# Performance work log

Measured on AMD Instinct MI355X. Metric: run time of the kernel, lower is better.

The kernel has to match this reference:

```python
import jax, jax.numpy as jnp
import numpy as np

# Config (BERT-base with T5-style shared relative attention bias)
B, S, D, H, F, V, L = 16, 512, 768, 12, 3072, 30522, 12
DH = D // H
MAXREL = 128  # bias table has 2*MAXREL+1 = 257 buckets
EPS = 1e-12


def layer_norm(x, w, b):
    mu = jnp.mean(x, axis=-1, keepdims=True)
    var = jnp.mean(jnp.square(x - mu), axis=-1, keepdims=True)
    return (x - mu) * jax.lax.rsqrt(var + EPS) * w + b


def setup_inputs() -> dict:
    key = jax.random.key(0)
    ks = jax.random.split(key, 16)
    s = 0.02
    inp = {
        "input_ids": jax.random.randint(ks[0], (B, S), 0, V),
        "attention_mask": jnp.ones((B, S), jnp.float32),
        "word_emb": jax.random.normal(ks[1], (V, D), jnp.float32) * s,
        "pos_emb": jax.random.normal(ks[2], (S, D), jnp.float32) * s,
        "emb_ln_w": jnp.ones((D,), jnp.float32),
        "emb_ln_b": jnp.zeros((D,), jnp.float32),
        "rel_bias_table": jax.random.normal(ks[3], (2 * MAXREL + 1, H), jnp.float32) * s,
        "Wq": jax.random.normal(ks[4], (L, D, D), jnp.float32) * s,
        "bq": jnp.zeros((L, D), jnp.float32),
        "Wk": jax.random.normal(ks[5], (L, D, D), jnp.float32) * s,
        "bk": jnp.zeros((L, D), jnp.float32),
        "Wv": jax.random.normal(ks[6], (L, D, D), jnp.float32) * s,
        "bv": jnp.zeros((L, D), jnp.float32),
        "Wo": jax.random.normal(ks[7], (L, D, D), jnp.float32) * s,
        "bo": jnp.zeros((L, D), jnp.float32),
        "attn_ln_w": jnp.ones((L, D), jnp.float32),
        "attn_ln_b": jnp.zeros((L, D), jnp.float32),
        "Wi": jax.random.normal(ks[8], (L, F, D), jnp.float32) * s,
        "bi": jnp.zeros((L, F), jnp.float32),
        "Wd": jax.random.normal(ks[9], (L, D, F), jnp.float32) * s,
        "bd": jnp.zeros((L, D), jnp.float32),
        "out_ln_w": jnp.ones((L, D), jnp.float32),
        "out_ln_b": jnp.zeros((L, D), jnp.float32),
    }
    return inp


def _encoder(input_ids, attention_mask, word_emb, pos_emb, emb_ln_w, emb_ln_b,
             rel_bias_table, Wq, bq, Wk, bk, Wv, bv, Wo, bo, attn_ln_w, attn_ln_b,
             Wi, bi, Wd, bd, out_ln_w, out_ln_b):
    b, s = input_ids.shape
    # Embeddings: word + learned absolute position, then LayerNorm
    h = word_emb[input_ids] + pos_emb[:s][None, :, :]
    h = layer_norm(h, emb_ln_w, emb_ln_b)

    # Shared relative position bias: [H, S, S]
    pos = jnp.arange(s)
    rel = jnp.clip(pos[None, :] - pos[:, None], -MAXREL, MAXREL) + MAXREL
    rel_bias = jnp.transpose(rel_bias_table[rel], (2, 0, 1))[None]  # [1,H,S,S]

    # Additive attention mask: [B,1,1,S]
    add_mask = (1.0 - attention_mask)[:, None, None, :] * -10000.0
    scale = 1.0 / np.sqrt(DH)

    def step(h, p):
        wq, bq_, wk, bk_, wv, bv_, wo, bo_, lw1, lb1, wi, bi_, wd, bd_, lw2, lb2 = p
        q = (h @ wq.T + bq_).reshape(b, s, H, DH)
        k = (h @ wk.T + bk_).reshape(b, s, H, DH)
        v = (h @ wv.T + bv_).reshape(b, s, H, DH)
        scores = jnp.einsum('bqhd,bkhd->bhqk', q, k) * scale + rel_bias + add_mask
        attn = jax.nn.softmax(scores, axis=-1)
        ctx = jnp.einsum('bhqk,bkhd->bqhd', attn, v).reshape(b, s, D)
        h1 = layer_norm(h + (ctx @ wo.T + bo_), lw1, lb1)
        inter = jax.nn.gelu(h1 @ wi.T + bi_, approximate=False)
        h2 = layer_norm(h1 + (inter @ wd.T + bd_), lw2, lb2)
        return h2, None

    params = (Wq, bq, Wk, bk, Wv, bv, Wo, bo, attn_ln_w, attn_ln_b,
              Wi, bi, Wd, bd, out_ln_w, out_ln_b)
    h, _ = jax.lax.scan(step, h, params)
    return h


def reference(input_ids, attention_mask, word_emb, pos_emb, emb_ln_w, emb_ln_b,
              rel_bias_table, Wq, bq, Wk, bk, Wv, bv, Wo, bo, attn_ln_w, attn_ln_b,
              Wi, bi, Wd, bd, out_ln_w, out_ln_b):
    return _encoder(input_ids, attention_mask, word_emb, pos_emb, emb_ln_w, emb_ln_b,
                    rel_bias_table, Wq, bq, Wk, bk, Wv, bv, Wo, bo, attn_ln_w, attn_ln_b,
                    Wi, bi, Wd, bd, out_ln_w, out_ln_b)
```

## Files before the change

kernel.cpp:

```cpp
#include <hip/hip_runtime.h>
#include <cstdint>
#include <cstddef>

#define BB 16
#define SS 512
#define DD 768
#define HH 12
#define FF 3072
#define LL 12
#define DHD 64
#define MM (BB*SS)

typedef __attribute__((ext_vector_type(8))) short bf16x8;
typedef __attribute__((ext_vector_type(4))) float f32x4;

__device__ __forceinline__ ushort f2bf(float f) {
  union { float f; uint32_t u; } x; x.f = f;
  uint32_t r = x.u + 0x7FFFu + ((x.u >> 16) & 1u);
  return (ushort)(r >> 16);
}

__device__ __forceinline__ void glds16(const ushort* g, ushort* l) {
  __builtin_amdgcn_global_load_lds((__attribute__((address_space(1))) void*)g,
                                   (__attribute__((address_space(3))) void*)l,
                                   16, 0, 0);
}

__device__ __forceinline__ float gelu_t(float v) {
  float y = 0.7978845608f * (v + 0.044715f * v * v * v);
  y = fminf(fmaxf(y, -15.f), 15.f);
  float e = __expf(2.f * y);
  return 0.5f * v * (2.f - 2.f / (e + 1.f));
}

__global__ __launch_bounds__(256)
void convw6(const float* __restrict__ s0, const float* __restrict__ s1,
            const float* __restrict__ s2, const float* __restrict__ s3,
            const float* __restrict__ s4, const float* __restrict__ s5,
            ushort* __restrict__ dA, ushort* __restrict__ dB, int perD, int perF)
{
  const int y = blockIdx.y;
  const int per = (y < 4) ? perD : perF;
  const int i = (blockIdx.x * 256 + threadIdx.x) * 4;
  if (i >= per) return;
  const float* s = y == 0 ? s0 : y == 1 ? s1 : y == 2 ? s2 : y == 3 ? s3 : y == 4 ? s4 : s5;
  ushort* dst = (y < 4) ? (dA + (size_t)y * perD) : (dB + (size_t)(y - 4) * perF);
  const float4 v = *(const float4*)(s + i);
  ushort4 o;
  o.x = f2bf(v.x); o.y = f2bf(v.y); o.z = f2bf(v.z); o.w = f2bf(v.w);
  *(ushort4*)(dst + i) = o;
}

__global__ __launch_bounds__(256)
void embed_ln_kernel(const int* __restrict__ ids, const float* __restrict__ wemb,
                     const float* __restrict__ pemb, const float* __restrict__ g,
                     const float* __restrict__ bt, float* __restrict__ hf,
                     ushort* __restrict__ hb)
{
  const int row = blockIdx.x;
  const int s = row & (SS - 1);
  const int id = ids[row];
  const float* wp = wemb + (size_t)id * DD;
  const float* pp = pemb + (size_t)s * DD;
  const int tid = threadIdx.x;
  float v[3]; float sum = 0.f, sq = 0.f;
#pragma unroll
  for (int j = 0; j < 3; ++j) {
    int e = tid + j * 256;
    v[j] = wp[e] + pp[e];
    sum += v[j]; sq += v[j] * v[j];
  }
  __shared__ float red[2][4];
#pragma unroll
  for (int off = 32; off >= 1; off >>= 1) { sum += __shfl_xor(sum, off); sq += __shfl_xor(sq, off); }
  const int lane = tid & 63, wid = tid >> 6;
  if (lane == 0) { red[0][wid] = sum; red[1][wid] = sq; }
  __syncthreads();
  sum = red[0][0] + red[0][1] + red[0][2] + red[0][3];
  sq  = red[1][0] + red[1][1] + red[1][2] + red[1][3];
  const float mean = sum * (1.f / DD);
  const float var  = sq  * (1.f / DD) - mean * mean;
  const float rstd = rsqrtf(var + 1e-12f);
  const size_t base = (size_t)row * DD;
#pragma unroll
  for (int j = 0; j < 3; ++j) {
    int e = tid + j * 256;
    float o = (v[j] - mean) * rstd * g[e] + bt[e];
    hf[base + e] = o;
    hb[base + e] = f2bf(o);
  }
}

__global__ __launch_bounds__(256)
void add_ln2_kernel(const float* __restrict__ res, const float* __restrict__ p0,
                    const float* __restrict__ p1, const float* __restrict__ g,
                    const float* __restrict__ bt, float* __restrict__ hf,
                    ushort* __restrict__ hb)
{
  const int row = blockIdx.x;
  const int tid = threadIdx.x;
  const size_t base = (size_t)row * DD;
  float v[3]; float sum = 0.f, sq = 0.f;
#pragma unroll
  for (int j = 0; j < 3; ++j) {
    int e = tid + j * 256;
    v[j] = res[base + e] + p0[base + e] + p1[base + e];
    sum += v[j]; sq += v[j] * v[j];
  }
  __shared__ float red[2][4];
#pragma unroll
  for (int off = 32; off >= 1; off >>= 1) { sum += __shfl_xor(sum, off); sq += __shfl_xor(sq, off); }
  const int lane = tid & 63, wid = tid >> 6;
  if (lane == 0) { red[0][wid] = sum; red[1][wid] = sq; }
  __syncthreads();
  sum = red[0][0] + red[0][1] + red[0][2] + red[0][3];
  sq  = red[1][0] + red[1][1] + red[1][2] + red[1][3];
  const float mean = sum * (1.f / DD);
  const float var  = sq  * (1.f / DD) - mean * mean;
  const float rstd = rsqrtf(var + 1e-12f);
#pragma unroll
  for (int j = 0; j < 3; ++j) {
    int e = tid + j * 256;
    float o = (v[j] - mean) * rstd * g[e] + bt[e];
    hf[base + e] = o;
    hb[base + e] = f2bf(o);
  }
}

template<int EPI, bool TRV>
__global__ __launch_bounds__(256, 4)
void gemm_ker(const ushort* __restrict__ A,
              const ushort* __restrict__ B0, const ushort* __restrict__ B1,
              const ushort* __restrict__ B2,
              const float* __restrict__ bias0, const float* __restrict__ bias1,
              const float* __restrict__ bias2,
              void* __restrict__ C0, void* __restrict__ C1, void* __restrict__ C2,
              int Kdim, int nblk)
{
  __shared__ ushort As[2][128 * 32];
  __shared__ ushort Bs[2][128 * 32];

  int id = blockIdx.y * gridDim.x + blockIdx.x;
  const int chunk = (gridDim.x * gridDim.y) >> 3;
  id = (id & 7) * chunk + (id >> 3);
  const int bm = id & 63;
  const int bnAll = id >> 6;
  const int sub = bnAll / nblk;
  const int bn = bnAll - sub * nblk;

  const ushort* Bw  = sub == 0 ? B0 : (sub == 1 ? B1 : B2);
  const float* bias = sub == 0 ? bias0 : (sub == 1 ? bias1 : bias2);
  const int Ndim = nblk * 128;

  const int tid = threadIdx.x;
  const int l = tid & 63, w = tid >> 6;
  const int wm = w >> 1, wn = w & 1;
  const int fr = l & 15, fg = l >> 4;

  const int srow_in = l >> 2;
  const int gks = ((l & 3) ^ ((l >> 3) & 3)) * 8;
  const ushort* Agl0 = A  + (size_t)(bm * 128 + w * 16 + srow_in) * Kdim + gks;
  const ushort* Agl1 = Agl0 + (size_t)64 * Kdim;
  const ushort* Bgl0 = Bw + (size_t)(bn * 128 + w * 16 + srow_in) * Kdim + gks;
  const ushort* Bgl1 = Bgl0 + (size_t)64 * Kdim;

  auto stage = [&](int b, int kt) {
    const int ko = kt * 32;
    ushort* al = &As[b][w * 64 * 8];
    ushort* bl = &Bs[b][w * 64 * 8];
    glds16(Agl0 + ko, al);
    glds16(Agl1 + ko, al + 256 * 8);
    glds16(Bgl0 + ko, bl);
    glds16(Bgl1 + ko, bl + 256 * 8);
  };

  const int se = (fg ^ ((fr >> 1) & 3)) * 8;

  f32x4 acc[4][4];
#pragma unroll
  for (int i = 0; i < 4; ++i)
#pragma unroll
    for (int j = 0; j < 4; ++j) acc[i][j] = f32x4{0.f, 0.f, 0.f, 0.f};

  stage(0, 0);
  __syncthreads();

  const int nk = Kdim >> 5;
  int cur = 0;
  for (int kt = 0; kt < nk; ++kt) {
    if (kt + 1 < nk) stage(cur ^ 1, kt + 1);

    bf16x8 af[4], bfv[4];
#pragma unroll
    for (int i = 0; i < 4; ++i)
      af[i]  = *(const bf16x8*)&As[cur][(wm * 64 + i * 16 + fr) * 32 + se];
#pragma unroll
    for (int j = 0; j < 4; ++j)
      bfv[j] = *(const bf16x8*)&Bs[cur][(wn * 64 + j * 16 + fr) * 32 + se];

    __builtin_amdgcn_s_setprio(1);
#pragma unroll
    for (int i = 0; i < 4; ++i)
#pragma unroll
      for (int j = 0; j < 4; ++j)
        acc[i][j] = __builtin_amdgcn_mfma_f32_16x16x32_bf16(bfv[j], af[i], acc[i][j], 0, 0, 0);
    __builtin_amdgcn_s_setprio(0);

    __syncthreads();
    cur ^= 1;
  }

#pragma unroll
  for (int i = 0; i < 4; ++i) {
    const int row_g = bm * 128 + wm * 64 + i * 16 + fr;
#pragma unroll
    for (int j = 0; j < 4; ++j) {
      const int col = bn * 128 + wn * 64 + j * 16 + fg * 4;
      const float4 bv4 = *(const float4*)&bias[col];
      const float v0 = acc[i][j][0] + bv4.x;
      const float v1 = acc[i][j][1] + bv4.y;
      const float v2 = acc[i][j][2] + bv4.z;
      const float v3 = acc[i][j][3] + bv4.w;
      if (TRV && sub == 2) {
        const int b_ = row_g >> 9, s_ = row_g & 511;
        const int h_ = col >> 6, d0 = col & 63;
        ushort* vp = (ushort*)C2 + (((size_t)(b_ * HH + h_) * DHD + d0) * SS + s_);
        vp[0] = f2bf(v0); vp[SS] = f2bf(v1); vp[2 * SS] = f2bf(v2); vp[3 * SS] = f2bf(v3);
      } else if (EPI == 2) {
        ushort4 o4;
        o4.x = f2bf(gelu_t(v0)); o4.y = f2bf(gelu_t(v1));
        o4.z = f2bf(gelu_t(v2)); o4.w = f2bf(gelu_t(v3));
        *(ushort4*)&((ushort*)C0)[(size_t)row_g * Ndim + col] = o4;
      } else {
        void* Cout = sub == 0 ? C0 : (sub == 1 ? C1 : C2);
        ushort4 o4;
        o4.x = f2bf(v0); o4.y = f2bf(v1); o4.z = f2bf(v2); o4.w = f2bf(v3);
        *(ushort4*)&((ushort*)Cout)[(size_t)row_g * Ndim + col] = o4;
      }
    }
  }
}

__global__ __launch_bounds__(256, 4)
void gemm_sk(const ushort* __restrict__ A, const ushort* __restrict__ Bw,
             const float* __restrict__ bias, float* __restrict__ P0,
             float* __restrict__ P1, int Kdim)
{
  __shared__ ushort As[2][128 * 32];
  __shared__ ushort Bs[2][128 * 32];

  int id = blockIdx.y * gridDim.x + blockIdx.x;
  const int chunk = (gridDim.x * gridDim.y) >> 3;
  id = (id & 7) * chunk + (id >> 3);
  const int bm = id & 63;
  const int rest = id >> 6;
  const int bn = rest >> 1;
  const int sk = rest & 1;

  const int Kh = Kdim >> 1;

  const int tid = threadIdx.x;
  const int l = tid & 63, w = tid >> 6;
  const int wm = w >> 1, wn = w & 1;
  const int fr = l & 15, fg = l >> 4;

  const int srow_in = l >> 2;
  const int gks = ((l & 3) ^ ((l >> 3) & 3)) * 8;
  const ushort* Agl0 = A  + (size_t)(bm * 128 + w * 16 + srow_in) * Kdim + sk * Kh + gks;
  const ushort* Agl1 = Agl0 + (size_t)64 * Kdim;
  const ushort* Bgl0 = Bw + (size_t)(bn * 128 + w * 16 + srow_in) * Kdim + sk * Kh + gks;
  const ushort* Bgl1 = Bgl0 + (size_t)64 * Kdim;

  auto stage = [&](int b, int kt) {
    const int ko = kt * 32;
    ushort* al = &As[b][w * 64 * 8];
    ushort* bl = &Bs[b][w * 64 * 8];
    glds16(Agl0 + ko, al);
    glds16(Agl1 + ko, al + 256 * 8);
    glds16(Bgl0 + ko, bl);
    glds16(Bgl1 + ko, bl + 256 * 8);
  };

  const int se = (fg ^ ((fr >> 1) & 3)) * 8;

  f32x4 acc[4][4];
#pragma unroll
  for (int i = 0; i < 4; ++i)
#pragma unroll
    for (int j = 0; j < 4; ++j) acc[i][j] = f32x4{0.f, 0.f, 0.f, 0.f};

  stage(0, 0);
  __syncthreads();

  const int nk = Kh >> 5;
  int cur = 0;
  for (int kt = 0; kt < nk; ++kt) {
    if (kt + 1 < nk) stage(cur ^ 1, kt + 1);

    bf16x8 af[4], bfv[4];
#pragma unroll
    for (int i = 0; i < 4; ++i)
      af[i]  = *(const bf16x8*)&As[cur][(wm * 64 + i * 16 + fr) * 32 + se];
#pragma unroll
    for (int j = 0; j < 4; ++j)
      bfv[j] = *(const bf16x8*)&Bs[cur][(wn * 64 + j * 16 + fr) * 32 + se];

    __builtin_amdgcn_s_setprio(1);
#pragma unroll
    for (int i = 0; i < 4; ++i)
#pragma unroll
      for (int j = 0; j < 4; ++j)
        acc[i][j] = __builtin_amdgcn_mfma_f32_16x16x32_bf16(bfv[j], af[i], acc[i][j], 0, 0, 0);
    __builtin_amdgcn_s_setprio(0);

    __syncthreads();
    cur ^= 1;
  }

  float* P = sk ? P1 : P0;
  const float bs = sk ? 0.f : 1.f;
#pragma unroll
  for (int i = 0; i < 4; ++i) {
    const int row_g = bm * 128 + wm * 64 + i * 16 + fr;
#pragma unroll
    for (int j = 0; j < 4; ++j) {
      const int col = bn * 128 + wn * 64 + j * 16 + fg * 4;
      const float4 bv4 = *(const float4*)&bias[col];
      float4 o4;
      o4.x = acc[i][j][0] + bv4.x * bs;
      o4.y = acc[i][j][1] + bv4.y * bs;
      o4.z = acc[i][j][2] + bv4.z * bs;
      o4.w = acc[i][j][3] + bv4.w * bs;
      *(float4*)&P[(size_t)row_g * DD + col] = o4;
    }
  }
}

__global__ __launch_bounds__(256, 3)
void attn_kernel(const ushort* __restrict__ qb, const ushort* __restrict__ kb,
                 const ushort* __restrict__ vt, const float* __restrict__ relt,
                 const float* __restrict__ amask, ushort* __restrict__ ctxb)
{
  __shared__ ushort Kt[128][72];
  __shared__ ushort Vt[64][136];
  __shared__ ushort Pl[64][136];
  __shared__ float am_lds[512];
  __shared__ float rel_lds[1024];

  const int tid = threadIdx.x, lane = tid & 63, w = tid >> 6;

  int lin = blockIdx.y * gridDim.x + blockIdx.x;
  lin = (lin & 7) * 192 + (lin >> 3);
  const int qt = lin & 7;
  const int bh = lin >> 3;
  const int b = bh / HH, h = bh - b * HH;
  const int fr = lane & 15, fg = lane >> 4;

  for (int i = tid; i < 512; i += 256)
    am_lds[i] = (1.0f - amask[b * SS + i]) * -10000.0f;
  for (int i = tid; i < 1024; i += 256) {
    int d = i - 512;
    d = min(128, max(-128, d));
    rel_lds[i] = relt[(d + 128) * HH + h];
  }

  bf16x8 qf[2];
  {
    const int qrow = qt * 64 + w * 16 + fr;
    const ushort* p = qb + ((size_t)(b * SS + qrow) * DD) + h * DHD + fg * 8;
    qf[0] = *(const bf16x8*)p;
    qf[1] = *(const bf16x8*)(p + 32);
  }

  f32x4 o[4];
  float mrow[4], lrow[4];
#pragma unroll
  for (int r = 0; r < 4; ++r) { mrow[r] = -1e30f; lrow[r] = 0.f; }
#pragma unroll
  for (int d = 0; d < 4; ++d) o[d] = f32x4{0.f, 0.f, 0.f, 0.f};

  const int skr = tid >> 1;
  const int shd = (tid & 1) * 32;
  const int vrow = tid >> 2;
  const int vcg  = (tid & 3) * 32;
  const ushort* vgl = vt + ((size_t)bh * DHD + vrow) * SS + vcg;

  const int qg0 = qt * 64 + w * 16;

  for (int kt = 0; kt < 4; ++kt) {
    const size_t gbase = ((size_t)(b * SS + kt * 128 + skr) * DD) + h * DHD + shd;
    int4 kr0 = *(const int4*)(kb + gbase);
    int4 kr1 = *(const int4*)(kb + gbase + 8);
    int4 kr2 = *(const int4*)(kb + gbase + 16);
    int4 kr3 = *(const int4*)(kb + gbase + 24);
    const ushort* vp = vgl + kt * 128;
    int4 vr0 = *(const int4*)(vp);
    int4 vr1 = *(const int4*)(vp + 8);
    int4 vr2 = *(const int4*)(vp + 16);
    int4 vr3 = *(const int4*)(vp + 24);

    __syncthreads();
    *(int4*)&Kt[skr][shd]      = kr0;
    *(int4*)&Kt[skr][shd + 8]  = kr1;
    *(int4*)&Kt[skr][shd + 16] = kr2;
    *(int4*)&Kt[skr][shd + 24] = kr3;
    *(int4*)&Vt[vrow][vcg]      = vr0;
    *(int4*)&Vt[vrow][vcg + 8]  = vr1;
    *(int4*)&Vt[vrow][vcg + 16] = vr2;
    *(int4*)&Vt[vrow][vcg + 24] = vr3;
    __syncthreads();

    float sv[8][4];
    __builtin_amdgcn_s_setprio(1);
#pragma unroll
    for (int kc = 0; kc < 8; ++kc) {
      f32x4 s = f32x4{0.f, 0.f, 0.f, 0.f};
      bf16x8 kf0 = *(const bf16x8*)&Kt[kc * 16 + fr][fg * 8];
      bf16x8 kf1 = *(const bf16x8*)&Kt[kc * 16 + fr][32 + fg * 8];
      s = __builtin_amdgcn_mfma_f32_16x16x32_bf16(qf[0], kf0, s, 0, 0, 0);
      s = __builtin_amdgcn_mfma_f32_16x16x32_bf16(qf[1], kf1, s, 0, 0, 0);
      const int col = kt * 128 + kc * 16 + fr;
      const float am = am_lds[col];
      const int ridx = col - qg0 - fg * 4 + 512;
#pragma unroll
      for (int r = 0; r < 4; ++r)
        sv[kc][r] = s[r] * 0.125f + rel_lds[ridx - r] + am;
    }
    __builtin_amdgcn_s_setprio(0);

    float ef[4];
#pragma unroll
    for (int r = 0; r < 4; ++r) {
      float tmax = sv[0][r];
#pragma unroll
      for (int kc = 1; kc < 8; ++kc) tmax = fmaxf(tmax, sv[kc][r]);
#pragma unroll
      for (int off = 1; off < 16; off <<= 1) tmax = fmaxf(tmax, __shfl_xor(tmax, off));
      const float mnew = fmaxf(mrow[r], tmax);
      ef[r] = __expf(mrow[r] - mnew);
      float psum = 0.f;
      const int prow = w * 16 + fg * 4 + r;
#pragma unroll
      for (int kc = 0; kc < 8; ++kc) {
        float p = __expf(sv[kc][r] - mnew);
        psum += p;
        Pl[prow][kc * 16 + fr] = f2bf(p);
      }
#pragma unroll
      for (int off = 1; off < 16; off <<= 1) psum += __shfl_xor(psum, off);
      lrow[r] = lrow[r] * ef[r] + psum;
      mrow[r] = mnew;
    }
#pragma unroll
    for (int dc = 0; dc < 4; ++dc)
#pragma unroll
      for (int r = 0; r < 4; ++r) o[dc][r] *= ef[r];
    __syncthreads();

    __builtin_amdgcn_s_setprio(1);
#pragma unroll
    for (int dc = 0; dc < 4; ++dc)
#pragma unroll
      for (int ks = 0; ks < 4; ++ks) {
        bf16x8 pf = *(const bf16x8*)&Pl[w * 16 + fr][ks * 32 + fg * 8];
        bf16x8 vf = *(const bf16x8*)&Vt[dc * 16 + fr][ks * 32 + fg * 8];
        o[dc] = __builtin_amdgcn_mfma_f32_16x16x32_bf16(pf, vf, o[dc], 0, 0, 0);
      }
    __builtin_amdgcn_s_setprio(0);
  }

#pragma unroll
  for (int dc = 0; dc < 4; ++dc)
#pragma unroll
    for (int r = 0; r < 4; ++r) {
      const int qg = qt * 64 + w * 16 + fg * 4 + r;
      const float v = o[dc][r] / lrow[r];
      ctxb[((size_t)(b * SS + qg) * DD) + h * DHD + dc * 16 + fr] = f2bf(v);
    }
}

extern "C" void kernel_launch(void* const* d_in, const int* in_sizes, int n_in,
                              void* d_out, int out_size, void* d_ws, size_t ws_size,
                              hipStream_t stream) {
  const int*   ids   = (const int*)d_in[0];
  const float* amask = (const float*)d_in[1];
  const float* wemb  = (const float*)d_in[2];
  const float* pemb  = (const float*)d_in[3];
  const float* eln_w = (const float*)d_in[4];
  const float* eln_b = (const float*)d_in[5];
  const float* relt  = (const float*)d_in[6];
  const float* Wq    = (const float*)d_in[7];
  const float* bq    = (const float*)d_in[8];
  const float* Wk    = (const float*)d_in[9];
  const float* bk    = (const float*)d_in[10];
  const float* Wv    = (const float*)d_in[11];
  const float* bv    = (const float*)d_in[12];
  const float* Wo    = (const float*)d_in[13];
  const float* bo    = (const float*)d_in[14];
  const float* aln_w = (const float*)d_in[15];
  const float* aln_b = (const float*)d_in[16];
  const float* Wi    = (const float*)d_in[17];
  const float* bi    = (const float*)d_in[18];
  const float* Wd    = (const float*)d_in[19];
  const float* bd    = (const float*)d_in[20];
  const float* oln_w = (const float*)d_in[21];
  const float* oln_b = (const float*)d_in[22];

  size_t off = 0;
  auto carve = [&](size_t bytes) -> void* {
    void* r = (char*)d_ws + off;
    off += (bytes + 255) & ~(size_t)255;
    return r;
  };
  float*  hf     = (float*) carve((size_t)MM * DD * 4);
  ushort* hb     = (ushort*)carve((size_t)MM * DD * 2);
  ushort* qbuf   = (ushort*)carve((size_t)MM * DD * 2);
  ushort* kbuf   = (ushort*)carve((size_t)MM * DD * 2);
  ushort* vbuf   = (ushort*)carve((size_t)MM * DD * 2);
  ushort* ctxb   = (ushort*)carve((size_t)MM * DD * 2);
  float*  gout   = (float*) carve((size_t)MM * DD * 4);
  float*  gout2  = (float*) carve((size_t)MM * DD * 4);
  ushort* interb = (ushort*)carve((size_t)MM * FF * 2);
  const int PD = DD * DD;
  const int PF = FF * DD;
  ushort* wBded  = (ushort*)carve((size_t)2 * PF * 2);

  ushort* wA = interb;

  embed_ln_kernel<<<MM, 256, 0, stream>>>(ids, wemb, pemb, eln_w, eln_b, hf, hb);

  const dim3 gQKV(MM / 128, 3 * (DD / 128));
  const dim3 gSK(MM / 128, 2 * (DD / 128));
  const dim3 gF(MM / 128, FF / 128);
  const dim3 gA(SS / 64, BB * HH);
  const dim3 gC(PF / 1024, 6);

  for (int l = 0; l < LL; ++l) {
    const size_t wo  = (size_t)l * PD;
    const size_t wio = (size_t)l * PF;

    convw6<<<gC, 256, 0, stream>>>(Wq + wo, Wk + wo, Wv + wo, Wo + wo,
                                   Wi + wio, Wd + wio, wA, wBded, PD, PF);

    gemm_ker<0, true><<<gQKV, 256, 0, stream>>>(hb, wA, wA + PD, wA + 2 * PD,
                                                bq + l * DD, bk + l * DD, bv + l * DD,
                                                qbuf, kbuf, vbuf, DD, DD / 128);

    attn_kernel<<<gA, 256, 0, stream>>>(qbuf, kbuf, vbuf, relt, amask, ctxb);

    gemm_sk<<<gSK, 256, 0, stream>>>(ctxb, wA + 3 * PD, bo + l * DD, gout, gout2, DD);
    add_ln2_kernel<<<MM, 256, 0, stream>>>(hf, gout, gout2,
                                           aln_w + l * DD, aln_b + l * DD, hf, hb);

    gemm_ker<2, false><<<gF, 256, 0, stream>>>(hb, wBded, wBded, wBded,
                                               bi + l * FF, bi + l * FF, bi + l * FF,
                                               interb, interb, interb, DD, FF / 128);
    gemm_sk<<<gSK, 256, 0, stream>>>(interb, wBded + PF, bd + l * DD, gout, gout2, FF);

    float* outp = (l == LL - 1) ? (float*)d_out : hf;
    add_ln2_kernel<<<MM, 256, 0, stream>>>(hf, gout, gout2,
                                           oln_w + l * DD, oln_b + l * DD, outp, hb);
  }
}
```

Measured before the change: 3.600 ms.

## Store split-K partials as bf16, enlarge attention tiles, simplify GELU

The split-K GEMM partial outputs are now written and read as bf16 instead of fp32, halving the bytes that move between gemm_sk and the add+LayerNorm kernel. The attention kernel now uses 512 threads and 128-query tiles, so each K/V tile is shared by twice as many queries and there are half as many blocks. The tanh-GELU is rewritten in sigmoid form with one exp and no clamp. The risks are the extra rounding from bf16 partial sums before the residual add, and lower occupancy or LDS pressure in the bigger attention blocks.

```diff
diff --git a/kernel.cpp b/kernel.cpp
--- a/kernel.cpp
+++ b/kernel.cpp
@@ -19,6 +19,10 @@
   uint32_t r = x.u + 0x7FFFu + ((x.u >> 16) & 1u);
   return (ushort)(r >> 16);
 }
+__device__ __forceinline__ float bf2f(ushort u) {
+  union { uint32_t u; float f; } x; x.u = (uint32_t)u << 16;
+  return x.f;
+}
 
 __device__ __forceinline__ void glds16(const ushort* g, ushort* l) {
   __builtin_amdgcn_global_load_lds((__attribute__((address_space(1))) void*)g,
@@ -27,10 +31,9 @@
 }
 
 __device__ __forceinline__ float gelu_t(float v) {
-  float y = 0.7978845608f * (v + 0.044715f * v * v * v);
-  y = fminf(fmaxf(y, -15.f), 15.f);
-  float e = __expf(2.f * y);
-  return 0.5f * v * (2.f - 2.f / (e + 1.f));
+  const float v2 = v * v;
+  const float u = v * (-1.5957691216f - 0.0713548163f * v2);
+  return v / (1.f + __expf(u));
 }
 
 __global__ __launch_bounds__(256)
@@ -92,8 +95,8 @@
 }
 
 __global__ __launch_bounds__(256)
-void add_ln2_kernel(const float* __restrict__ res, const float* __restrict__ p0,
-                    const float* __restrict__ p1, const float* __restrict__ g,
+void add_ln2_kernel(const float* __restrict__ res, const ushort* __restrict__ p0,
+                    const ushort* __restrict__ p1, const float* __restrict__ g,
                     const float* __restrict__ bt, float* __restrict__ hf,
                     ushort* __restrict__ hb)
 {
@@ -104,7 +107,7 @@
 #pragma unroll
   for (int j = 0; j < 3; ++j) {
     int e = tid + j * 256;
-    v[j] = res[base + e] + p0[base + e] + p1[base + e];
+    v[j] = res[base + e] + bf2f(p0[base + e]) + bf2f(p1[base + e]);
     sum += v[j]; sq += v[j] * v[j];
   }
   __shared__ float red[2][4];
@@ -243,8 +246,8 @@
 
 __global__ __launch_bounds__(256, 4)
 void gemm_sk(const ushort* __restrict__ A, const ushort* __restrict__ Bw,
-             const float* __restrict__ bias, float* __restrict__ P0,
-             float* __restrict__ P1, int Kdim)
+             const float* __restrict__ bias, ushort* __restrict__ P0,
+             ushort* __restrict__ P1, int Kdim)
 {
   __shared__ ushort As[2][128 * 32];
   __shared__ ushort Bs[2][128 * 32];
@@ -317,7 +320,7 @@
     cur ^= 1;
   }
 
-  float* P = sk ? P1 : P0;
+  ushort* P = sk ? P1 : P0;
   const float bs = sk ? 0.f : 1.f;
 #pragma unroll
   for (int i = 0; i < 4; ++i) {
@@ -326,47 +329,49 @@
     for (int j = 0; j < 4; ++j) {
       const int col = bn * 128 + wn * 64 + j * 16 + fg * 4;
       const float4 bv4 = *(const float4*)&bias[col];
-      float4 o4;
-      o4.x = acc[i][j][0] + bv4.x * bs;
-      o4.y = acc[i][j][1] + bv4.y * bs;
-      o4.z = acc[i][j][2] + bv4.z * bs;
-      o4.w = acc[i][j][3] + bv4.w * bs;
-      *(float4*)&P[(size_t)row_g * DD + col] = o4;
+      ushort4 o4;
+      o4.x = f2bf(acc[i][j][0] + bv4.x * bs);
+      o4.y = f2bf(acc[i][j][1] + bv4.y * bs);
+      o4.z = f2bf(acc[i][j][2] + bv4.z * bs);
+      o4.w = f2bf(acc[i][j][3] + bv4.w * bs);
+      *(ushort4*)&P[(size_t)row_g * DD + col] = o4;
     }
   }
 }
 
-__global__ __launch_bounds__(256, 3)
+__global__ __launch_bounds__(512, 2)
 void attn_kernel(const ushort* __restrict__ qb, const ushort* __restrict__ kb,
                  const ushort* __restrict__ vt, const float* __restrict__ relt,
                  const float* __restrict__ amask, ushort* __restrict__ ctxb)
 {
   __shared__ ushort Kt[128][72];
   __shared__ ushort Vt[64][136];
-  __shared__ ushort Pl[64][136];
+  __shared__ ushort Pl[128][136];
   __shared__ float am_lds[512];
   __shared__ float rel_lds[1024];
 
   const int tid = threadIdx.x, lane = tid & 63, w = tid >> 6;
 
   int lin = blockIdx.y * gridDim.x + blockIdx.x;
-  lin = (lin & 7) * 192 + (lin >> 3);
-  const int qt = lin & 7;
-  const int bh = lin >> 3;
+  lin = (lin & 7) * 96 + (lin >> 3);
+  const int qt = lin & 3;
+  const int bh = lin >> 2;
   const int b = bh / HH, h = bh - b * HH;
   const int fr = lane & 15, fg = lane >> 4;
 
-  for (int i = tid; i < 512; i += 256)
-    am_lds[i] = (1.0f - amask[b * SS + i]) * -10000.0f;
-  for (int i = tid; i < 1024; i += 256) {
-    int d = i - 512;
-    d = min(128, max(-128, d));
-    rel_lds[i] = relt[(d + 128) * HH + h];
+  am_lds[tid] = (1.0f - amask[b * SS + tid]) * -10000.0f;
+  {
+    int d0 = tid - 512;
+    d0 = max(-128, d0);
+    rel_lds[tid] = relt[(d0 + 128) * HH + h];
+    int d1 = tid;
+    d1 = min(128, d1);
+    rel_lds[tid + 512] = relt[(d1 + 128) * HH + h];
   }
 
   bf16x8 qf[2];
   {
-    const int qrow = qt * 64 + w * 16 + fr;
+    const int qrow = qt * 128 + w * 16 + fr;
     const ushort* p = qb + ((size_t)(b * SS + qrow) * DD) + h * DHD + fg * 8;
     qf[0] = *(const bf16x8*)p;
     qf[1] = *(const bf16x8*)(p + 32);
@@ -379,35 +384,27 @@
 #pragma unroll
   for (int d = 0; d < 4; ++d) o[d] = f32x4{0.f, 0.f, 0.f, 0.f};
 
-  const int skr = tid >> 1;
-  const int shd = (tid & 1) * 32;
-  const int vrow = tid >> 2;
-  const int vcg  = (tid & 3) * 32;
+  const int skr = tid >> 2;
+  const int shd = (tid & 3) * 16;
+  const int vrow = tid >> 3;
+  const int vcg  = (tid & 7) * 16;
   const ushort* vgl = vt + ((size_t)bh * DHD + vrow) * SS + vcg;
 
-  const int qg0 = qt * 64 + w * 16;
+  const int qg0 = qt * 128 + w * 16;
 
   for (int kt = 0; kt < 4; ++kt) {
     const size_t gbase = ((size_t)(b * SS + kt * 128 + skr) * DD) + h * DHD + shd;
     int4 kr0 = *(const int4*)(kb + gbase);
     int4 kr1 = *(const int4*)(kb + gbase + 8);
-    int4 kr2 = *(const int4*)(kb + gbase + 16);
-    int4 kr3 = *(const int4*)(kb + gbase + 24);
     const ushort* vp = vgl + kt * 128;
     int4 vr0 = *(const int4*)(vp);
     int4 vr1 = *(const int4*)(vp + 8);
-    int4 vr2 = *(const int4*)(vp + 16);
-    int4 vr3 = *(const int4*)(vp + 24);
 
     __syncthreads();
-    *(int4*)&Kt[skr][shd]      = kr0;
-    *(int4*)&Kt[skr][shd + 8]  = kr1;
-    *(int4*)&Kt[skr][shd + 16] = kr2;
-    *(int4*)&Kt[skr][shd + 24] = kr3;
-    *(int4*)&Vt[vrow][vcg]      = vr0;
-    *(int4*)&Vt[vrow][vcg + 8]  = vr1;
-    *(int4*)&Vt[vrow][vcg + 16] = vr2;
-    *(int4*)&Vt[vrow][vcg + 24] = vr3;
+    *(int4*)&Kt[skr][shd]     = kr0;
+    *(int4*)&Kt[skr][shd + 8] = kr1;
+    *(int4*)&Vt[vrow][vcg]     = vr0;
+    *(int4*)&Vt[vrow][vcg + 8] = vr1;
     __syncthreads();
 
     float sv[8][4];
@@ -473,7 +470,7 @@
   for (int dc = 0; dc < 4; ++dc)
 #pragma unroll
     for (int r = 0; r < 4; ++r) {
-      const int qg = qt * 64 + w * 16 + fg * 4 + r;
+      const int qg = qt * 128 + w * 16 + fg * 4 + r;
       const float v = o[dc][r] / lrow[r];
       ctxb[((size_t)(b * SS + qg) * DD) + h * DHD + dc * 16 + fr] = f2bf(v);
     }
@@ -518,8 +515,8 @@
   ushort* kbuf   = (ushort*)carve((size_t)MM * DD * 2);
   ushort* vbuf   = (ushort*)carve((size_t)MM * DD * 2);
   ushort* ctxb   = (ushort*)carve((size_t)MM * DD * 2);
-  float*  gout   = (float*) carve((size_t)MM * DD * 4);
-  float*  gout2  = (float*) carve((size_t)MM * DD * 4);
+  ushort* gout   = (ushort*)carve((size_t)MM * DD * 2);
+  ushort* gout2  = (ushort*)carve((size_t)MM * DD * 2);
   ushort* interb = (ushort*)carve((size_t)MM * FF * 2);
   const int PD = DD * DD;
   const int PF = FF * DD;
@@ -532,7 +529,7 @@
   const dim3 gQKV(MM / 128, 3 * (DD / 128));
   const dim3 gSK(MM / 128, 2 * (DD / 128));
   const dim3 gF(MM / 128, FF / 128);
-  const dim3 gA(SS / 64, BB * HH);
+  const dim3 gA(SS / 128, BB * HH);
   const dim3 gC(PF / 1024, 6);
 
   for (int l = 0; l < LL; ++l) {
@@ -546,7 +543,7 @@
                                                 bq + l * DD, bk + l * DD, bv + l * DD,
                                                 qbuf, kbuf, vbuf, DD, DD / 128);
 
-    attn_kernel<<<gA, 256, 0, stream>>>(qbuf, kbuf, vbuf, relt, amask, ctxb);
+    attn_kernel<<<gA, 512, 0, stream>>>(qbuf, kbuf, vbuf, relt, amask, ctxb);
 
     gemm_sk<<<gSK, 256, 0, stream>>>(ctxb, wA + 3 * PD, bo + l * DD, gout, gout2, DD);
     add_ln2_kernel<<<MM, 256, 0, stream>>>(hf, gout, gout2,
```

Result: faster. 3.355 ms (-6.8%).
